# Optimization experiments

Measured on AMD Instinct MI355X. Metric: run time of the kernel, lower is better.

## Reference

```python
import jax, jax.numpy as jnp
import numpy as np

N_NODES = 100000
N_EDGES = 1600000
IN_DIM = 128
HID = 64
N_CLASSES = 40
NEG_SLOPE = 0.2


def setup_inputs() -> dict:
    key = jax.random.key(0)
    ks = jax.random.split(key, 12)
    s_in = 1.0 / np.sqrt(IN_DIM)
    s_h = 1.0 / np.sqrt(HID)
    return {
        "x": jax.random.normal(ks[0], (N_NODES, IN_DIM), dtype=jnp.float32),
        "edge_index": jax.random.randint(ks[1], (2, N_EDGES), 0, N_NODES, dtype=jnp.int64),
        "W0": jax.random.normal(ks[2], (IN_DIM, HID), dtype=jnp.float32) * s_in,
        "a_s0": jax.random.normal(ks[3], (HID,), dtype=jnp.float32) * s_h,
        "a_d0": jax.random.normal(ks[4], (HID,), dtype=jnp.float32) * s_h,
        "b0": jnp.zeros((HID,), dtype=jnp.float32),
        "W1": jax.random.normal(ks[5], (HID, HID), dtype=jnp.float32) * s_h,
        "a_s1": jax.random.normal(ks[6], (HID,), dtype=jnp.float32) * s_h,
        "a_d1": jax.random.normal(ks[7], (HID,), dtype=jnp.float32) * s_h,
        "b1": jnp.zeros((HID,), dtype=jnp.float32),
        "Wl": jax.random.normal(ks[8], (HID, N_CLASSES), dtype=jnp.float32) * s_h,
        "bl": jnp.zeros((N_CLASSES,), dtype=jnp.float32),
    }


def gat_conv(x, src, dst, W, a_s, a_d, b, n_nodes):
    # single-head GATConv (PyG default heads=1), self-loops already in src/dst
    h = x @ W                                  # [N, d]
    e = jax.nn.leaky_relu((h @ a_s)[src] + (h @ a_d)[dst], NEG_SLOPE)  # [E]
    # segment softmax over incoming edges of each dst node
    m = jax.ops.segment_max(e, dst, num_segments=n_nodes)
    p = jnp.exp(e - m[dst])
    denom = jax.ops.segment_sum(p, dst, num_segments=n_nodes)
    alpha = p / (denom[dst] + 1e-16)           # [E]
    out = jax.ops.segment_sum(alpha[:, None] * h[src], dst, num_segments=n_nodes)
    return out + b


def reference(x, edge_index, W0, a_s0, a_d0, b0, W1, a_s1, a_d1, b1, Wl, bl):
    n = x.shape[0]
    loop = jnp.arange(n, dtype=edge_index.dtype)
    src = jnp.concatenate([edge_index[0], loop])
    dst = jnp.concatenate([edge_index[1], loop])
    h = gat_conv(x, src, dst, W0, a_s0, a_d0, b0, n)
    h = jax.nn.elu(h)
    h = gat_conv(h, src, dst, W1, a_s1, a_d1, b1, n)
    h = jax.nn.elu(h)
    return h @ Wl + bl
```

## Files before the change

kernel.cpp:

```cpp
#include <hip/hip_runtime.h>
#include <math.h>

#define NEG_SLOPE 0.2f
#define CAP 256
#define BSH 9
#define BSZ 512
#define CHUNK 4096
#define PADS 16
#define CAPQ 16384

typedef __attribute__((ext_vector_type(8))) short short8;
typedef __attribute__((ext_vector_type(4))) float f32x4;

__device__ __forceinline__ float hred_sum(float v) {
#pragma unroll
    for (int o = 16; o >= 1; o >>= 1) v += __shfl_xor(v, o, 64);
    return v;
}
__device__ __forceinline__ unsigned int f2bf(float f) {
    unsigned int u = __float_as_uint(f);
    return (u + 0x7fffu + ((u >> 16) & 1u)) >> 16;
}
__device__ __forceinline__ float bflo(unsigned int u) { return __uint_as_float(u << 16); }
__device__ __forceinline__ float bfhi(unsigned int u) { return __uint_as_float(u & 0xffff0000u); }


__global__ __launch_bounds__(256) void k_scatter(
        const int* __restrict__ src, const int* __restrict__ dst,
        int* __restrict__ bcursor, int* __restrict__ ebuf, int E) {
    __shared__ int lh[256], lb[256];
    const int tid = threadIdx.x;
    int base = blockIdx.x * CHUNK;
    int sv[16], dv[16];
    bool ok[16];
#pragma unroll
    for (int u = 0; u < 16; ++u) {
        int i = base + u * 256 + tid;
        ok[u] = i < E;
        int ii = ok[u] ? i : E - 1;
        dv[u] = dst[ii];
        sv[u] = src[ii];
    }
    lh[tid] = 0;
    __syncthreads();
#pragma unroll
    for (int u = 0; u < 16; ++u)
        if (ok[u]) atomicAdd(&lh[dv[u] >> BSH], 1);
    __syncthreads();
    int c = lh[tid];
    lb[tid] = c ? atomicAdd(&bcursor[tid * PADS], c) : 0;
    lh[tid] = 0;
    __syncthreads();
#pragma unroll
    for (int u = 0; u < 16; ++u) {
        if (ok[u]) {
            int d = dv[u], b = d >> BSH;
            int pp = atomicAdd(&lh[b], 1);
            int pos = lb[b] + pp;
            if (pos < CAPQ)
                ebuf[b * CAPQ + pos] = (sv[u] << BSH) | (d & (BSZ - 1));
        }
    }
}


__device__ __forceinline__ void gemm0_body(char* smem, int bid,
        const float* __restrict__ X, const float* __restrict__ W,
        const float* __restrict__ a_s, const float* __restrict__ a_d,
        unsigned int* __restrict__ hb, float* __restrict__ ss, float* __restrict__ sd, int N) {
    constexpr int K = 128, OUTW = 64, NKC = K / 32, NC = OUTW / 16;
    short* wfrag = (short*)smem;
    unsigned int* hs = (unsigned int*)(smem + 16384);

    const int tid  = threadIdx.x;
    const int lane = tid & 63;
    const int w    = tid >> 6;
    const int m    = lane & 15;
    const int q8   = lane >> 4;
    const int rowbase = bid * 128 + w * 16;

    for (int f = tid; f < NKC * NC * 64; f += 512) {
        int flane = f & 63;
        int fc    = (f >> 6) % NC;
        int fkc   = (f >> 6) / NC;
        int col   = fc * 16 + (flane & 15);
        int k0    = fkc * 32 + (flane >> 4) * 8;
        short8 b;
#pragma unroll
        for (int j = 0; j < 8; ++j) b[j] = (short)f2bf(W[(k0 + j) * OUTW + col]);
        *(short8*)&wfrag[f * 8] = b;
    }
    __syncthreads();

    int grow = rowbase + m; if (grow >= N) grow = N - 1;

    f32x4 acc[NC];
#pragma unroll
    for (int c = 0; c < NC; ++c) acc[c] = (f32x4)0.f;

    const float* xrow = X + (size_t)grow * K + q8 * 8;
#pragma unroll
    for (int kc = 0; kc < NKC; ++kc) {
        float4 v0 = *(const float4*)(xrow + kc * 32);
        float4 v1 = *(const float4*)(xrow + kc * 32 + 4);
        float vv[8] = {v0.x, v0.y, v0.z, v0.w, v1.x, v1.y, v1.z, v1.w};
        short8 ah, al;
#pragma unroll
        for (int j = 0; j < 8; ++j) {
            unsigned int hb16 = f2bf(vv[j]);
            ah[j] = (short)hb16;
            al[j] = (short)f2bf(vv[j] - __uint_as_float(hb16 << 16));
        }
#pragma unroll
        for (int c = 0; c < NC; ++c) {
            short8 b = *(short8*)&wfrag[((kc * NC + c) * 64 + lane) * 8];
            acc[c] = __builtin_amdgcn_mfma_f32_16x16x32_bf16(ah, b, acc[c], 0, 0, 0);
            acc[c] = __builtin_amdgcn_mfma_f32_16x16x32_bf16(al, b, acc[c], 0, 0, 0);
        }
    }

    float asv[NC], adv[NC];
#pragma unroll
    for (int c = 0; c < NC; ++c) { asv[c] = a_s[c * 16 + m]; adv[c] = a_d[c * 16 + m]; }
#pragma unroll
    for (int i = 0; i < 4; ++i) {
        float s = 0.f, d = 0.f;
#pragma unroll
        for (int c = 0; c < NC; ++c) {
            s = fmaf(acc[c][i], asv[c], s);
            d = fmaf(acc[c][i], adv[c], d);
        }
#pragma unroll
        for (int o = 1; o <= 8; o <<= 1) {
            s += __shfl_xor(s, o, 64);
            d += __shfl_xor(d, o, 64);
        }
        int r = rowbase + q8 * 4 + i;
        if (m == 0 && r < N) { ss[r] = s; sd[r] = d; }
    }

    unsigned short* hsw = (unsigned short*)&hs[w * 512];
#pragma unroll
    for (int c = 0; c < NC; ++c)
#pragma unroll
        for (int i = 0; i < 4; ++i)
            hsw[(q8 * 4 + i) * 64 + c * 16 + m] = (unsigned short)f2bf(acc[c][i]);
    unsigned int* hu = &hs[w * 512];
    int row = lane >> 2, u0 = (lane & 3) * 8;
    uint4 va = *(uint4*)&hu[row * 32 + u0];
    uint4 vb = *(uint4*)&hu[row * 32 + u0 + 4];
    int r = rowbase + row;
    if (r < N) {
        *(uint4*)&hb[(size_t)r * 32 + u0]     = va;
        *(uint4*)&hb[(size_t)r * 32 + u0 + 4] = vb;
    }
}

__device__ __forceinline__ void build_body(char* smem, int b,
        const int* __restrict__ bcursor, const int* __restrict__ ebuf,
        int* __restrict__ rowptr, int* __restrict__ csr,
        int N, int nbuck) {
    int* sdeg  = (int*)smem;
    int* sscan = sdeg + 512;
    int* shdr  = sscan + 512;
    const int t = threadIdx.x;

    int nlo = b << BSH;
    int cn = N - nlo; if (cn > BSZ) cn = BSZ;

    int bcv = 0, totv = 0;
    if (t < 256) {
        int cnb = 0;
        if (t < nbuck) {
            bcv = bcursor[t * PADS]; if (bcv > CAPQ) bcv = CAPQ;
            cnb = N - (t << BSH); if (cnb > BSZ) cnb = BSZ; if (cnb < 0) cnb = 0;
        }
        totv = bcv + cnb;
        sscan[t] = totv;
    }
    __syncthreads();
#pragma unroll
    for (int off = 1; off < 256; off <<= 1) {
        int u = 0;
        if (t < 256 && t >= off) u = sscan[t - off];
        __syncthreads();
        if (t < 256) sscan[t] += u;
        __syncthreads();
    }
    if (t == b) { shdr[0] = sscan[t] - totv; shdr[1] = bcv; }
    if (b == 0 && t == nbuck - 1) rowptr[N] = sscan[t];
    __syncthreads();
    int cb = shdr[0], ec = shdr[1];
    int e0 = b * CAPQ;

    sdeg[t] = (t < cn) ? 1 : 0;
    __syncthreads();
    {
        int i = t;
        for (; i + 1536 < ec; i += 2048) {
            int r0 = ebuf[e0 + i], r1 = ebuf[e0 + i + 512];
            int r2 = ebuf[e0 + i + 1024], r3 = ebuf[e0 + i + 1536];
            atomicAdd(&sdeg[r0 & (BSZ - 1)], 1);
            atomicAdd(&sdeg[r1 & (BSZ - 1)], 1);
            atomicAdd(&sdeg[r2 & (BSZ - 1)], 1);
            atomicAdd(&sdeg[r3 & (BSZ - 1)], 1);
        }
        for (; i < ec; i += 512)
            atomicAdd(&sdeg[ebuf[e0 + i] & (BSZ - 1)], 1);
    }
    __syncthreads();
    int v = sdeg[t];
    sscan[t] = v;
    __syncthreads();
#pragma unroll
    for (int off = 1; off < BSZ; off <<= 1) {
        int u = (t >= off) ? sscan[t - off] : 0;
        __syncthreads();
        sscan[t] += u;
        __syncthreads();
    }
    int excl = sscan[t] - v;
    if (t < cn) {
        rowptr[nlo + t] = cb + excl;
        csr[cb + excl] = nlo + t;
        sdeg[t] = excl + 1;
    }
    __syncthreads();
    {
        int i = t;
        for (; i + 1536 < ec; i += 2048) {
            int r0 = ebuf[e0 + i], r1 = ebuf[e0 + i + 512];
            int r2 = ebuf[e0 + i + 1024], r3 = ebuf[e0 + i + 1536];
            int p0 = atomicAdd(&sdeg[r0 & (BSZ - 1)], 1);
            int p1 = atomicAdd(&sdeg[r1 & (BSZ - 1)], 1);
            int p2 = atomicAdd(&sdeg[r2 & (BSZ - 1)], 1);
            int p3 = atomicAdd(&sdeg[r3 & (BSZ - 1)], 1);
            csr[cb + p0] = r0 >> BSH;
            csr[cb + p1] = r1 >> BSH;
            csr[cb + p2] = r2 >> BSH;
            csr[cb + p3] = r3 >> BSH;
        }
        for (; i < ec; i += 512) {
            int rec = ebuf[e0 + i];
            int p = atomicAdd(&sdeg[rec & (BSZ - 1)], 1);
            csr[cb + p] = rec >> BSH;
        }
    }
}

__global__ __launch_bounds__(512) void k_mid(
        int* __restrict__ bcursor, int* __restrict__ ebuf, int gbm, int nbuck,
        const float* __restrict__ X, const float* __restrict__ W,
        const float* __restrict__ a_s, const float* __restrict__ a_d,
        unsigned int* __restrict__ hb, float* __restrict__ ss, float* __restrict__ sd,
        int* __restrict__ rowptr, int* __restrict__ csr, int N) {
    __shared__ __align__(16) char smem[32768];
    int bid = blockIdx.x;
    if (bid < gbm)
        gemm0_body(smem, bid, X, W, a_s, a_d, hb, ss, sd, N);
    else
        build_body(smem, bid - gbm, bcursor, ebuf, rowptr, csr, N, nbuck);
}


template <int K, int OUTW, bool SS, bool HB, bool XB>
__global__ __launch_bounds__(256) void k_gemm(const void* __restrict__ X,
                                              const float* __restrict__ W,
                                              const float* __restrict__ a_s,
                                              const float* __restrict__ a_d,
                                              const float* __restrict__ bias,
                                              void* __restrict__ Hout,
                                              float* __restrict__ ss,
                                              float* __restrict__ sd, int N) {
    constexpr int NKC = K / 32;
    constexpr int NC  = (OUTW + 15) / 16;
    __shared__ __align__(16) short wfrag[NKC * NC * 64 * 8];
    __shared__ __align__(16) unsigned int hs[HB ? 4 : 1][16 * 32];

    const int tid  = threadIdx.x;
    const int lane = tid & 63;
    const int w    = tid >> 6;
    const int m    = lane & 15;
    const int q8   = lane >> 4;
    const int rowbase = blockIdx.x * 64 + w * 16;

    for (int f = tid; f < NKC * NC * 64; f += 256) {
        int flane = f & 63;
        int fc    = (f >> 6) % NC;
        int fkc   = (f >> 6) / NC;
        int col   = fc * 16 + (flane & 15);
        int k0    = fkc * 32 + (flane >> 4) * 8;
        short8 b;
#pragma unroll
        for (int j = 0; j < 8; ++j) {
            float v = (col < OUTW) ? W[(k0 + j) * OUTW + col] : 0.f;
            b[j] = (short)f2bf(v);
        }
        *(short8*)&wfrag[f * 8] = b;
    }
    __syncthreads();

    int grow = rowbase + m; if (grow >= N) grow = N - 1;

    f32x4 acc[NC];
#pragma unroll
    for (int c = 0; c < NC; ++c) acc[c] = (f32x4)0.f;

    if (XB) {
        const unsigned short* xrow = (const unsigned short*)X + (size_t)grow * 64 + q8 * 8;
#pragma unroll
        for (int kc = 0; kc < NKC; ++kc) {
            short8 ah = *(const short8*)(xrow + kc * 32);
#pragma unroll
            for (int c = 0; c < NC; ++c) {
                short8 b = *(short8*)&wfrag[((kc * NC + c) * 64 + lane) * 8];
                acc[c] = __builtin_amdgcn_mfma_f32_16x16x32_bf16(ah, b, acc[c], 0, 0, 0);
            }
        }
    } else {
        const float* xrow = (const float*)X + (size_t)grow * K + q8 * 8;
#pragma unroll
        for (int kc = 0; kc < NKC; ++kc) {
            float4 v0 = *(const float4*)(xrow + kc * 32);
            float4 v1 = *(const float4*)(xrow + kc * 32 + 4);
            float vv[8] = {v0.x, v0.y, v0.z, v0.w, v1.x, v1.y, v1.z, v1.w};
            short8 ah, al;
#pragma unroll
            for (int j = 0; j < 8; ++j) {
                unsigned int hb16 = f2bf(vv[j]);
                ah[j] = (short)hb16;
                al[j] = (short)f2bf(vv[j] - __uint_as_float(hb16 << 16));
            }
#pragma unroll
            for (int c = 0; c < NC; ++c) {
                short8 b = *(short8*)&wfrag[((kc * NC + c) * 64 + lane) * 8];
                acc[c] = __builtin_amdgcn_mfma_f32_16x16x32_bf16(ah, b, acc[c], 0, 0, 0);
                acc[c] = __builtin_amdgcn_mfma_f32_16x16x32_bf16(al, b, acc[c], 0, 0, 0);
            }
        }
    }

    if (SS) {
        float asv[NC], adv[NC];
#pragma unroll
        for (int c = 0; c < NC; ++c) { asv[c] = a_s[c * 16 + m]; adv[c] = a_d[c * 16 + m]; }
#pragma unroll
        for (int i = 0; i < 4; ++i) {
            float s = 0.f, d = 0.f;
#pragma unroll
            for (int c = 0; c < NC; ++c) {
                s = fmaf(acc[c][i], asv[c], s);
                d = fmaf(acc[c][i], adv[c], d);
            }
#pragma unroll
            for (int o = 1; o <= 8; o <<= 1) {
                s += __shfl_xor(s, o, 64);
                d += __shfl_xor(d, o, 64);
            }
            int r = rowbase + q8 * 4 + i;
            if (m == 0 && r < N) { ss[r] = s; sd[r] = d; }
        }
    }

    if (HB) {
        unsigned short* hsw = (unsigned short*)&hs[w][0];
#pragma unroll
        for (int c = 0; c < NC; ++c)
#pragma unroll
            for (int i = 0; i < 4; ++i)
                hsw[(q8 * 4 + i) * 64 + c * 16 + m] = (unsigned short)f2bf(acc[c][i]);
        unsigned int* hu = &hs[w][0];
        int row = lane >> 2, u0 = (lane & 3) * 8;
        uint4 va = *(uint4*)&hu[row * 32 + u0];
        uint4 vb = *(uint4*)&hu[row * 32 + u0 + 4];
        int r = rowbase + row;
        if (r < N) {
            unsigned int* hbp = (unsigned int*)Hout;
            *(uint4*)&hbp[(size_t)r * 32 + u0]     = va;
            *(uint4*)&hbp[(size_t)r * 32 + u0 + 4] = vb;
        }
    } else {
        float bv[NC];
#pragma unroll
        for (int c = 0; c < NC; ++c) {
            int col = c * 16 + m;
            bv[c] = (col < OUTW) ? bias[col] : 0.f;
        }
        float* O = (float*)Hout;
#pragma unroll
        for (int i = 0; i < 4; ++i) {
            int r = rowbase + q8 * 4 + i;
            if (r < N) {
#pragma unroll
                for (int c = 0; c < NC; ++c) {
                    int col = c * 16 + m;
                    if (col < OUTW) O[(size_t)r * OUTW + col] = acc[c][i] + bv[c];
                }
            }
        }
    }
}


__global__ __launch_bounds__(256) void k_agg(const int* __restrict__ rowptr, const int* __restrict__ csr,
                                             const float* __restrict__ ss, const float* __restrict__ sd,
                                             const unsigned int* __restrict__ hb, const float* __restrict__ bias,
                                             unsigned int* __restrict__ z, int N) {
    __shared__ __align__(16) float sal[8][CAP];
    __shared__ __align__(16) int   sof[8][CAP];
    const int tid = threadIdx.x;
    const int hw  = tid >> 5;
    const int p   = tid & 31;
    const int n   = blockIdx.x * 8 + hw;
    const bool valid = n < N;
    const char* hbb = (const char*)hb;
    const int p4 = p * 4;

    int ro = 0, deg = 0;
    float sdn = 0.f;
    if (valid) {
        ro  = rowptr[n];
        deg = rowptr[n + 1] - ro;
        sdn = sd[n];
    }

    if (deg <= CAP) {
        float sum = 0.f;
        for (int j = p; j < deg; j += 32) {
            int s = csr[ro + j];
            float e = ss[s] + sdn;
            e = fmaxf(e, NEG_SLOPE * e);
            float pe = __expf(e);
            sal[hw][j] = pe;
            sof[hw][j] = s << 7;
            sum += pe;
        }
        sum = hred_sum(sum);
        float inv = 1.f / (sum + 1e-16f);

        float ax = 0.f, ay = 0.f, bx = 0.f, by = 0.f, cx = 0.f, cy = 0.f, dx = 0.f, dy = 0.f;
        int j = 0;
        for (; j + 7 < deg; j += 8) {
            float4 al0 = *(const float4*)&sal[hw][j];
            float4 al1 = *(const float4*)&sal[hw][j + 4];
            int4   of0 = *(const int4*)&sof[hw][j];
            int4   of1 = *(const int4*)&sof[hw][j + 4];
            unsigned int u0 = *(const unsigned int*)(hbb + (of0.x + p4));
            unsigned int u1 = *(const unsigned int*)(hbb + (of0.y + p4));
            unsigned int u2 = *(const unsigned int*)(hbb + (of0.z + p4));
            unsigned int u3 = *(const unsigned int*)(hbb + (of0.w + p4));
            unsigned int u4 = *(const unsigned int*)(hbb + (of1.x + p4));
            unsigned int u5 = *(const unsigned int*)(hbb + (of1.y + p4));
            unsigned int u6 = *(const unsigned int*)(hbb + (of1.z + p4));
            unsigned int u7 = *(const unsigned int*)(hbb + (of1.w + p4));
            ax = fmaf(bflo(u0), al0.x, ax); ay = fmaf(bfhi(u0), al0.x, ay);
            bx = fmaf(bflo(u1), al0.y, bx); by = fmaf(bfhi(u1), al0.y, by);
            cx = fmaf(bflo(u2), al0.z, cx); cy = fmaf(bfhi(u2), al0.z, cy);
            dx = fmaf(bflo(u3), al0.w, dx); dy = fmaf(bfhi(u3), al0.w, dy);
            ax = fmaf(bflo(u4), al1.x, ax); ay = fmaf(bfhi(u4), al1.x, ay);
            bx = fmaf(bflo(u5), al1.y, bx); by = fmaf(bfhi(u5), al1.y, by);
            cx = fmaf(bflo(u6), al1.z, cx); cy = fmaf(bfhi(u6), al1.z, cy);
            dx = fmaf(bflo(u7), al1.w, dx); dy = fmaf(bfhi(u7), al1.w, dy);
        }
        for (; j + 3 < deg; j += 4) {
            float4 al0 = *(const float4*)&sal[hw][j];
            int4   of0 = *(const int4*)&sof[hw][j];
            unsigned int u0 = *(const unsigned int*)(hbb + (of0.x + p4));
            unsigned int u1 = *(const unsigned int*)(hbb + (of0.y + p4));
            unsigned int u2 = *(const unsigned int*)(hbb + (of0.z + p4));
            unsigned int u3 = *(const unsigned int*)(hbb + (of0.w + p4));
            ax = fmaf(bflo(u0), al0.x, ax); ay = fmaf(bfhi(u0), al0.x, ay);
            bx = fmaf(bflo(u1), al0.y, bx); by = fmaf(bfhi(u1), al0.y, by);
            cx = fmaf(bflo(u2), al0.z, cx); cy = fmaf(bfhi(u2), al0.z, cy);
            dx = fmaf(bflo(u3), al0.w, dx); dy = fmaf(bfhi(u3), al0.w, dy);
        }
        for (; j < deg; ++j) {
            float a = sal[hw][j];
            unsigned int u0 = *(const unsigned int*)(hbb + (sof[hw][j] + p4));
            ax = fmaf(bflo(u0), a, ax); ay = fmaf(bfhi(u0), a, ay);
        }
        float fx = (ax + bx) + (cx + dx);
        float fy = (ay + by) + (cy + dy);
        if (valid) {
            float2 ob = *(const float2*)&bias[p * 2];
            float ox = fmaf(fx, inv, ob.x);
            float oy = fmaf(fy, inv, ob.y);
            ox = (ox > 0.f) ? ox : __expf(ox) - 1.f;
            oy = (oy > 0.f) ? oy : __expf(oy) - 1.f;
            z[(size_t)n * 32 + p] = (f2bf(oy) << 16) | f2bf(ox);
        }
    } else {
        float sum = 0.f;
        for (int j = p; j < deg; j += 32) {
            int s = csr[ro + j];
            float e = ss[s] + sdn;
            e = fmaxf(e, NEG_SLOPE * e);
            sum += __expf(e);
        }
        sum = hred_sum(sum);
        float inv = 1.f / (sum + 1e-16f);
        float fx = 0.f, fy = 0.f;
        for (int j = 0; j < deg; ++j) {
            int s = csr[ro + j];
            float e = ss[s] + sdn;
            e = fmaxf(e, NEG_SLOPE * e);
            float pe = __expf(e);
            unsigned int u = *(const unsigned int*)(hbb + ((s << 7) + p4));
            fx = fmaf(bflo(u), pe, fx); fy = fmaf(bfhi(u), pe, fy);
        }
        float2 ob = *(const float2*)&bias[p * 2];
        float ox = fmaf(fx, inv, ob.x);
        float oy = fmaf(fy, inv, ob.y);
        ox = (ox > 0.f) ? ox : __expf(ox) - 1.f;
        oy = (oy > 0.f) ? oy : __expf(oy) - 1.f;
        z[(size_t)n * 32 + p] = (f2bf(oy) << 16) | f2bf(ox);
    }
}


extern "C" void kernel_launch(void* const* d_in, const int* in_sizes, int n_in,
                              void* d_out, int out_size, void* d_ws, size_t ws_size,
                              hipStream_t stream) {
    const float* x   = (const float*)d_in[0];
    const int*   ei  = (const int*)d_in[1];
    const float* W0  = (const float*)d_in[2];
    const float* as0 = (const float*)d_in[3];
    const float* ad0 = (const float*)d_in[4];
    const float* b0  = (const float*)d_in[5];
    const float* W1  = (const float*)d_in[6];
    const float* as1 = (const float*)d_in[7];
    const float* ad1 = (const float*)d_in[8];
    const float* b1  = (const float*)d_in[9];
    const float* Wl  = (const float*)d_in[10];
    const float* bl  = (const float*)d_in[11];
    float* out = (float*)d_out;

    int N = in_sizes[0] / 128;
    int E = in_sizes[1] / 2;
    const int* srcp = ei;
    const int* dstp = ei + E;
    int nbuck = (N + BSZ - 1) >> BSH;

    char* wp = (char*)d_ws;
    auto alloc = [&](size_t bytes) { void* p = (void*)wp; wp += (bytes + 255) & ~(size_t)255; return p; };
    unsigned int* hb = (unsigned int*)alloc((size_t)N * 32 * 4);
    unsigned int* z  = (unsigned int*)alloc((size_t)N * 32 * 4);
    float* ssb     = (float*)alloc((size_t)N * 4);
    float* sdb     = (float*)alloc((size_t)N * 4);
    int*   rowptr  = (int*)alloc((size_t)(N + 1) * 4);
    int*   csr     = (int*)alloc((size_t)(E + N) * 4);
    int*   ebuf    = (int*)alloc((size_t)nbuck * CAPQ * 4);
    int*   bcursor = (int*)alloc(256 * PADS * 4);

    int nscat = (E + CHUNK - 1) / CHUNK;
    int gbm = (N + 127) / 128;
    int gb2 = (N + 63) / 64;

    hipMemsetAsync(bcursor, 0, 256 * PADS * 4, stream);
    k_scatter<<<nscat, 256, 0, stream>>>(srcp, dstp, bcursor, ebuf, E);
    k_mid<<<gbm + nbuck, 512, 0, stream>>>(bcursor, ebuf, gbm, nbuck,
                                           x, W0, as0, ad0, hb, ssb, sdb,
                                           rowptr, csr, N);

    k_agg<<<(N + 7) / 8, 256, 0, stream>>>(rowptr, csr, ssb, sdb, hb, b0, z, N);
    k_gemm<64, 64, true, true, true><<<gb2, 256, 0, stream>>>(z, W1, as1, ad1, nullptr, hb, ssb, sdb, N);
    k_agg<<<(N + 7) / 8, 256, 0, stream>>>(rowptr, csr, ssb, sdb, hb, b1, z, N);
    k_gemm<64, 40, false, false, true><<<gb2, 256, 0, stream>>>(z, Wl, nullptr, nullptr, bl, out, nullptr, nullptr, N);
}
```

Baseline: 239.9 us.

## Fuse aggregation with following GEMM into single per-block kernel

Merges each aggregation kernel with the dense transform that follows it, so the block of 16 nodes writes its ELU'd bf16 features into shared-memory MFMA fragments and multiplies by W1 (or Wl) right away. This removes the round trip of the intermediate z buffer through global memory and two kernel launches. The layer-2 attention scores come from per-wave partials reduced in shared memory. CAP is halved to fit the larger blocks' shared memory, so more high-degree nodes take the slow uncached path, and separate ping-pong buffers are used since input and output can no longer alias.

```diff
diff --git a/kernel.cpp b/kernel.cpp
--- a/kernel.cpp
+++ b/kernel.cpp
@@ -2,7 +2,7 @@
 #include <math.h>
 
 #define NEG_SLOPE 0.2f
-#define CAP 256
+#define CAP 128
 #define BSH 9
 #define BSZ 512
 #define CHUNK 4096
@@ -263,28 +263,32 @@
 }
 
 
-template <int K, int OUTW, bool SS, bool HB, bool XB>
-__global__ __launch_bounds__(256) void k_gemm(const void* __restrict__ X,
-                                              const float* __restrict__ W,
-                                              const float* __restrict__ a_s,
-                                              const float* __restrict__ a_d,
-                                              const float* __restrict__ bias,
-                                              void* __restrict__ Hout,
-                                              float* __restrict__ ss,
-                                              float* __restrict__ sd, int N) {
-    constexpr int NKC = K / 32;
+template <int OUTW, bool LAST>
+__global__ __launch_bounds__(512) void k_aggmm(
+        const int* __restrict__ rowptr, const int* __restrict__ csr,
+        const float* __restrict__ ss, const float* __restrict__ sd,
+        const unsigned int* __restrict__ hb, const float* __restrict__ bias,
+        const float* __restrict__ W, const float* __restrict__ a_s2,
+        const float* __restrict__ a_d2,
+        unsigned int* __restrict__ hbout, float* __restrict__ ssout,
+        float* __restrict__ sdout,
+        const float* __restrict__ bias2, float* __restrict__ fout, int N) {
+    constexpr int NKC = 2;
     constexpr int NC  = (OUTW + 15) / 16;
     __shared__ __align__(16) short wfrag[NKC * NC * 64 * 8];
-    __shared__ __align__(16) unsigned int hs[HB ? 4 : 1][16 * 32];
+    __shared__ __align__(16) float sal[16][CAP];
+    __shared__ __align__(16) int   sof[16][CAP];
+    __shared__ __align__(16) short afrag[NKC][512];
+    __shared__ __align__(16) unsigned short hsw[LAST ? 1 : 16][64];
+    __shared__ float ssp[LAST ? 1 : NC][16], sdp[LAST ? 1 : NC][16];
 
     const int tid  = threadIdx.x;
     const int lane = tid & 63;
     const int w    = tid >> 6;
     const int m    = lane & 15;
     const int q8   = lane >> 4;
-    const int rowbase = blockIdx.x * 64 + w * 16;
-
-    for (int f = tid; f < NKC * NC * 64; f += 256) {
+
+    for (int f = tid; f < NKC * NC * 64; f += 512) {
         int flane = f & 63;
         int fc    = (f >> 6) % NC;
         int fkc   = (f >> 6) / NC;
@@ -298,120 +302,11 @@
         }
         *(short8*)&wfrag[f * 8] = b;
     }
-    __syncthreads();
-
-    int grow = rowbase + m; if (grow >= N) grow = N - 1;
-
-    f32x4 acc[NC];
-#pragma unroll
-    for (int c = 0; c < NC; ++c) acc[c] = (f32x4)0.f;
-
-    if (XB) {
-        const unsigned short* xrow = (const unsigned short*)X + (size_t)grow * 64 + q8 * 8;
-#pragma unroll
-        for (int kc = 0; kc < NKC; ++kc) {
-            short8 ah = *(const short8*)(xrow + kc * 32);
-#pragma unroll
-            for (int c = 0; c < NC; ++c) {
-                short8 b = *(short8*)&wfrag[((kc * NC + c) * 64 + lane) * 8];
-                acc[c] = __builtin_amdgcn_mfma_f32_16x16x32_bf16(ah, b, acc[c], 0, 0, 0);
-            }
-        }
-    } else {
-        const float* xrow = (const float*)X + (size_t)grow * K + q8 * 8;
-#pragma unroll
-        for (int kc = 0; kc < NKC; ++kc) {
-            float4 v0 = *(const float4*)(xrow + kc * 32);
-            float4 v1 = *(const float4*)(xrow + kc * 32 + 4);
-            float vv[8] = {v0.x, v0.y, v0.z, v0.w, v1.x, v1.y, v1.z, v1.w};
-            short8 ah, al;
-#pragma unroll
-            for (int j = 0; j < 8; ++j) {
-                unsigned int hb16 = f2bf(vv[j]);
-                ah[j] = (short)hb16;
-                al[j] = (short)f2bf(vv[j] - __uint_as_float(hb16 << 16));
-            }
-#pragma unroll
-            for (int c = 0; c < NC; ++c) {
-                short8 b = *(short8*)&wfrag[((kc * NC + c) * 64 + lane) * 8];
-                acc[c] = __builtin_amdgcn_mfma_f32_16x16x32_bf16(ah, b, acc[c], 0, 0, 0);
-                acc[c] = __builtin_amdgcn_mfma_f32_16x16x32_bf16(al, b, acc[c], 0, 0, 0);
-            }
-        }
-    }
-
-    if (SS) {
-        float asv[NC], adv[NC];
-#pragma unroll
-        for (int c = 0; c < NC; ++c) { asv[c] = a_s[c * 16 + m]; adv[c] = a_d[c * 16 + m]; }
-#pragma unroll
-        for (int i = 0; i < 4; ++i) {
-            float s = 0.f, d = 0.f;
-#pragma unroll
-            for (int c = 0; c < NC; ++c) {
-                s = fmaf(acc[c][i], asv[c], s);
-                d = fmaf(acc[c][i], adv[c], d);
-            }
-#pragma unroll
-            for (int o = 1; o <= 8; o <<= 1) {
-                s += __shfl_xor(s, o, 64);
-                d += __shfl_xor(d, o, 64);
-            }
-            int r = rowbase + q8 * 4 + i;
-            if (m == 0 && r < N) { ss[r] = s; sd[r] = d; }
-        }
-    }
-
-    if (HB) {
-        unsigned short* hsw = (unsigned short*)&hs[w][0];
-#pragma unroll
-        for (int c = 0; c < NC; ++c)
-#pragma unroll
-            for (int i = 0; i < 4; ++i)
-                hsw[(q8 * 4 + i) * 64 + c * 16 + m] = (unsigned short)f2bf(acc[c][i]);
-        unsigned int* hu = &hs[w][0];
-        int row = lane >> 2, u0 = (lane & 3) * 8;
-        uint4 va = *(uint4*)&hu[row * 32 + u0];
-        uint4 vb = *(uint4*)&hu[row * 32 + u0 + 4];
-        int r = rowbase + row;
-        if (r < N) {
-            unsigned int* hbp = (unsigned int*)Hout;
-            *(uint4*)&hbp[(size_t)r * 32 + u0]     = va;
-            *(uint4*)&hbp[(size_t)r * 32 + u0 + 4] = vb;
-        }
-    } else {
-        float bv[NC];
-#pragma unroll
-        for (int c = 0; c < NC; ++c) {
-            int col = c * 16 + m;
-            bv[c] = (col < OUTW) ? bias[col] : 0.f;
-        }
-        float* O = (float*)Hout;
-#pragma unroll
-        for (int i = 0; i < 4; ++i) {
-            int r = rowbase + q8 * 4 + i;
-            if (r < N) {
-#pragma unroll
-                for (int c = 0; c < NC; ++c) {
-                    int col = c * 16 + m;
-                    if (col < OUTW) O[(size_t)r * OUTW + col] = acc[c][i] + bv[c];
-                }
-            }
-        }
-    }
-}
-
-
-__global__ __launch_bounds__(256) void k_agg(const int* __restrict__ rowptr, const int* __restrict__ csr,
-                                             const float* __restrict__ ss, const float* __restrict__ sd,
-                                             const unsigned int* __restrict__ hb, const float* __restrict__ bias,
-                                             unsigned int* __restrict__ z, int N) {
-    __shared__ __align__(16) float sal[8][CAP];
-    __shared__ __align__(16) int   sof[8][CAP];
-    const int tid = threadIdx.x;
-    const int hw  = tid >> 5;
-    const int p   = tid & 31;
-    const int n   = blockIdx.x * 8 + hw;
+
+    const int hw = tid >> 5;
+    const int p  = tid & 31;
+    const int nb = blockIdx.x * 16;
+    const int n  = nb + hw;
     const bool valid = n < N;
     const char* hbb = (const char*)hb;
     const int p4 = p * 4;
@@ -424,6 +319,7 @@
         sdn = sd[n];
     }
 
+    float fxr, fyr, inv;
     if (deg <= CAP) {
         float sum = 0.f;
         for (int j = p; j < deg; j += 32) {
@@ -436,7 +332,7 @@
             sum += pe;
         }
         sum = hred_sum(sum);
-        float inv = 1.f / (sum + 1e-16f);
+        inv = 1.f / (sum + 1e-16f);
 
         float ax = 0.f, ay = 0.f, bx = 0.f, by = 0.f, cx = 0.f, cy = 0.f, dx = 0.f, dy = 0.f;
         int j = 0;
@@ -479,16 +375,8 @@
             unsigned int u0 = *(const unsigned int*)(hbb + (sof[hw][j] + p4));
             ax = fmaf(bflo(u0), a, ax); ay = fmaf(bfhi(u0), a, ay);
         }
-        float fx = (ax + bx) + (cx + dx);
-        float fy = (ay + by) + (cy + dy);
-        if (valid) {
-            float2 ob = *(const float2*)&bias[p * 2];
-            float ox = fmaf(fx, inv, ob.x);
-            float oy = fmaf(fy, inv, ob.y);
-            ox = (ox > 0.f) ? ox : __expf(ox) - 1.f;
-            oy = (oy > 0.f) ? oy : __expf(oy) - 1.f;
-            z[(size_t)n * 32 + p] = (f2bf(oy) << 16) | f2bf(ox);
-        }
+        fxr = (ax + bx) + (cx + dx);
+        fyr = (ay + by) + (cy + dy);
     } else {
         float sum = 0.f;
         for (int j = p; j < deg; j += 32) {
@@ -498,7 +386,7 @@
             sum += __expf(e);
         }
         sum = hred_sum(sum);
-        float inv = 1.f / (sum + 1e-16f);
+        inv = 1.f / (sum + 1e-16f);
         float fx = 0.f, fy = 0.f;
         for (int j = 0; j < deg; ++j) {
             int s = csr[ro + j];
@@ -508,12 +396,73 @@
             unsigned int u = *(const unsigned int*)(hbb + ((s << 7) + p4));
             fx = fmaf(bflo(u), pe, fx); fy = fmaf(bfhi(u), pe, fy);
         }
+        fxr = fx; fyr = fy;
+    }
+    {
         float2 ob = *(const float2*)&bias[p * 2];
-        float ox = fmaf(fx, inv, ob.x);
-        float oy = fmaf(fy, inv, ob.y);
+        float ox = fmaf(fxr, inv, ob.x);
+        float oy = fmaf(fyr, inv, ob.y);
         ox = (ox > 0.f) ? ox : __expf(ox) - 1.f;
         oy = (oy > 0.f) ? oy : __expf(oy) - 1.f;
-        z[(size_t)n * 32 + p] = (f2bf(oy) << 16) | f2bf(ox);
+        unsigned int zu = (f2bf(oy) << 16) | f2bf(ox);
+        int k   = 2 * p;
+        int kc  = k >> 5;
+        int idx = ((((k & 31) >> 3) * 16 + hw) << 3) + (k & 7);
+        *(unsigned int*)&afrag[kc][idx] = zu;
+    }
+    __syncthreads();
+
+    if (w < NC) {
+        f32x4 acc = (f32x4)0.f;
+#pragma unroll
+        for (int kc = 0; kc < NKC; ++kc) {
+            short8 a = *(short8*)&afrag[kc][lane * 8];
+            short8 b = *(short8*)&wfrag[((kc * NC + w) * 64 + lane) * 8];
+            acc = __builtin_amdgcn_mfma_f32_16x16x32_bf16(a, b, acc, 0, 0, 0);
+        }
+        if constexpr (LAST) {
+#pragma unroll
+            for (int i = 0; i < 4; ++i) {
+                int r = nb + q8 * 4 + i;
+                int col = w * 16 + m;
+                if (r < N && col < OUTW)
+                    fout[(size_t)r * OUTW + col] = acc[i] + bias2[col];
+            }
+        } else {
+            float asv = a_s2[w * 16 + m];
+            float adv = a_d2[w * 16 + m];
+#pragma unroll
+            for (int i = 0; i < 4; ++i) {
+                float s = acc[i] * asv, d = acc[i] * adv;
+#pragma unroll
+                for (int o = 1; o <= 8; o <<= 1) {
+                    s += __shfl_xor(s, o, 64);
+                    d += __shfl_xor(d, o, 64);
+                }
+                if (m == 0) { ssp[w][q8 * 4 + i] = s; sdp[w][q8 * 4 + i] = d; }
+                hsw[q8 * 4 + i][w * 16 + m] = (unsigned short)f2bf(acc[i]);
+            }
+        }
+    }
+    if constexpr (!LAST) {
+        __syncthreads();
+        if (tid < 16) {
+            int r = nb + tid;
+            if (r < N) {
+                float s = 0.f, d = 0.f;
+#pragma unroll
+                for (int c = 0; c < NC; ++c) { s += ssp[c][tid]; d += sdp[c][tid]; }
+                ssout[r] = s; sdout[r] = d;
+            }
+        }
+        if (tid < 128) {
+            int row = tid >> 3, seg = tid & 7;
+            int r = nb + row;
+            if (r < N) {
+                uint4 v = *(uint4*)&((unsigned int*)hsw)[row * 32 + seg * 4];
+                *(uint4*)&hbout[(size_t)r * 32 + seg * 4] = v;
+            }
+        }
     }
 }
 
@@ -543,10 +492,12 @@
 
     char* wp = (char*)d_ws;
     auto alloc = [&](size_t bytes) { void* p = (void*)wp; wp += (bytes + 255) & ~(size_t)255; return p; };
-    unsigned int* hb = (unsigned int*)alloc((size_t)N * 32 * 4);
-    unsigned int* z  = (unsigned int*)alloc((size_t)N * 32 * 4);
-    float* ssb     = (float*)alloc((size_t)N * 4);
-    float* sdb     = (float*)alloc((size_t)N * 4);
+    unsigned int* hb0 = (unsigned int*)alloc((size_t)N * 32 * 4);
+    unsigned int* hb1 = (unsigned int*)alloc((size_t)N * 32 * 4);
+    float* ss0     = (float*)alloc((size_t)N * 4);
+    float* sd0     = (float*)alloc((size_t)N * 4);
+    float* ss1     = (float*)alloc((size_t)N * 4);
+    float* sd1     = (float*)alloc((size_t)N * 4);
     int*   rowptr  = (int*)alloc((size_t)(N + 1) * 4);
     int*   csr     = (int*)alloc((size_t)(E + N) * 4);
     int*   ebuf    = (int*)alloc((size_t)nbuck * CAPQ * 4);
@@ -554,16 +505,18 @@
 
     int nscat = (E + CHUNK - 1) / CHUNK;
     int gbm = (N + 127) / 128;
-    int gb2 = (N + 63) / 64;
+    int gagg = (N + 15) / 16;
 
     hipMemsetAsync(bcursor, 0, 256 * PADS * 4, stream);
     k_scatter<<<nscat, 256, 0, stream>>>(srcp, dstp, bcursor, ebuf, E);
     k_mid<<<gbm + nbuck, 512, 0, stream>>>(bcursor, ebuf, gbm, nbuck,
-                                           x, W0, as0, ad0, hb, ssb, sdb,
+                                           x, W0, as0, ad0, hb0, ss0, sd0,
                                            rowptr, csr, N);
 
-    k_agg<<<(N + 7) / 8, 256, 0, stream>>>(rowptr, csr, ssb, sdb, hb, b0, z, N);
-    k_gemm<64, 64, true, true, true><<<gb2, 256, 0, stream>>>(z, W1, as1, ad1, nullptr, hb, ssb, sdb, N);
-    k_agg<<<(N + 7) / 8, 256, 0, stream>>>(rowptr, csr, ssb, sdb, hb, b1, z, N);
-    k_gemm<64, 40, false, false, true><<<gb2, 256, 0, stream>>>(z, Wl, nullptr, nullptr, bl, out, nullptr, nullptr, N);
-}
+    k_aggmm<64, false><<<gagg, 512, 0, stream>>>(rowptr, csr, ss0, sd0, hb0, b0,
+                                                 W1, as1, ad1,
+                                                 hb1, ss1, sd1, nullptr, nullptr, N);
+    k_aggmm<40, true><<<gagg, 512, 0, stream>>>(rowptr, csr, ss1, sd1, hb1, b1,
+                                                Wl, nullptr, nullptr,
+                                                nullptr, nullptr, nullptr, bl, out, N);
+}
```

After: 240.4 us. No clear change (+0.2%).
